# Kernel tuning notes

Measured on AMD Instinct MI355X. Metric: run time of the kernel, lower is better.

Reference implementation:

```python
import jax, jax.numpy as jnp
import numpy as np

TOP_K = 2


def setup_inputs() -> dict:
    key = jax.random.key(0)
    k0, k1, k2, k3, k4 = jax.random.split(key, 5)
    B, S, D, F, E = 4, 2048, 2048, 1408, 8
    scale = 0.02
    return {
        "hidden_states": jax.random.normal(k0, (B, S, D), jnp.float32),
        "router_w": jax.random.normal(k1, (D, E), jnp.float32) * scale,
        "w_gate": jax.random.normal(k2, (E, D, F), jnp.float32) * scale,
        "w_up": jax.random.normal(k3, (E, D, F), jnp.float32) * scale,
        "w_down": jax.random.normal(k4, (E, F, D), jnp.float32) * scale,
    }


def reference(hidden_states, router_w, w_gate, w_up, w_down):
    B, S, D = hidden_states.shape
    x = hidden_states.reshape(-1, D)              # [N, D]
    N = x.shape[0]
    E = router_w.shape[-1]

    # ---- Router: softmax over experts, top-k, renormalize top-k probs ----
    logits = x @ router_w                         # [N, E]
    probs = jax.nn.softmax(logits, axis=-1)
    top_w, top_i = jax.lax.top_k(probs, TOP_K)    # [N, K]
    top_w = top_w / jnp.sum(top_w, axis=-1, keepdims=True)

    # Dense gate matrix [N, E]: gate is the (renormalized) routing weight for
    # selected experts, zero otherwise.
    gates = jnp.zeros_like(probs).at[jnp.arange(N)[:, None], top_i].set(top_w)

    # ---- Load-balancing aux loss (Switch-style, averaged over top-k) ----
    f = jnp.mean(jnp.sum(jax.nn.one_hot(top_i, E, dtype=x.dtype), axis=1), axis=0)  # [E] dispatch fraction
    P = jnp.mean(probs, axis=0)                   # [E] mean router prob
    aux_loss = (E / TOP_K) * jnp.sum(f * P)

    # ---- Per-expert SwiGLU FFN, computed as grouped GEMMs over all experts ----
    g = jnp.einsum("nd,edf->enf", x, w_gate)      # [E, N, F]
    u = jnp.einsum("nd,edf->enf", x, w_up)        # [E, N, F]
    h = jax.nn.silu(g) * u                        # [E, N, F]
    expert_out = jnp.einsum("enf,efd->end", h, w_down)  # [E, N, D]

    # ---- Combine: gate-weighted sum over experts ----
    out = jnp.einsum("ne,end->nd", gates, expert_out)   # [N, D]
    return out.reshape(B, S, D), aux_loss
```

## Files before the change

kernel.cpp:

```cpp
#include <hip/hip_runtime.h>

#define N_TOK 8192
#define DIM   2048
#define FFN   1408

#define XB_OFF  0ull
#define HP_OFF  0ull
#define XGP_OFF 49020928ull
#define P1_OFF  120324096ull
#define EO_OFF  49020928ull
#define P2_OFF  212598784ull
#define LPK_OFF 258736128ull
#define TI_OFF  258801664ull
#define TW_OFF  258834432ull
#define TP_OFF  258867200ull
#define ST_OFF  258932736ull

typedef __bf16 bf16x8 __attribute__((ext_vector_type(8)));
typedef float  f32x4  __attribute__((ext_vector_type(4)));
typedef int    int4v  __attribute__((ext_vector_type(4)));
typedef __attribute__((address_space(1))) void as1_void;
typedef __attribute__((address_space(3))) void as3_void;

__device__ __forceinline__ void gload16(const void* g, void* l) {
  __builtin_amdgcn_global_load_lds((as1_void*)g, (as3_void*)l, 16, 0, 0);
}

__device__ __forceinline__ ushort f2bf(float f) {
  unsigned u = __builtin_bit_cast(unsigned, f);
  u += 0x7FFFu + ((u >> 16) & 1u);
  return (ushort)(u >> 16);
}

__device__ __forceinline__ int4v dsread(int addr) {
  int4v d;
  asm volatile("ds_read_b128 %0, %1" : "=v"(d) : "v"(addr));
  return d;
}

#define WAITL() do { asm volatile("s_waitcnt lgkmcnt(0)" ::: "memory"); \
                     __builtin_amdgcn_sched_barrier(0); } while (0)
#define BAR()   __builtin_amdgcn_s_barrier()
#define MFMA16(a, b, c) __builtin_amdgcn_mfma_f32_16x16x32_bf16(a, b, c, 0, 0, 0)
#define BC(x) __builtin_bit_cast(bf16x8, x)

__device__ __forceinline__ int swz(int row, int s) {
  int q = row >> 1;
  int p = (((row & 1) << 2) | s) ^ (q & 7);
  return q * 128 + p * 16;
}

__global__ __launch_bounds__(256) void router_kernel(
    const float* __restrict__ x, const float* __restrict__ rw,
    ushort* __restrict__ xb, int* __restrict__ topi, float* __restrict__ topw,
    int* __restrict__ cnt, unsigned long long* __restrict__ psum)
{
  int tid = threadIdx.x, lane = tid & 63, wv = tid >> 6;
  __shared__ float sP[4][8];
  __shared__ int   sC[4][8];
  float pacc[8]; int cacc[8];
  #pragma unroll
  for (int e = 0; e < 8; ++e) { pacc[e] = 0.f; cacc[e] = 0; }

  #pragma unroll 1
  for (int it = 0; it < 4; ++it) {
    int t = blockIdx.x * 16 + wv * 4 + it;
    const float4* xr = (const float4*)(x + (size_t)t * DIM);
    float acc[8];
    #pragma unroll
    for (int e = 0; e < 8; ++e) acc[e] = 0.f;
    #pragma unroll 1
    for (int i = 0; i < 8; ++i) {
      int j = i * 64 + lane;
      float4 v = xr[j];
      ushort4 o; o.x = f2bf(v.x); o.y = f2bf(v.y); o.z = f2bf(v.z); o.w = f2bf(v.w);
      *(ushort4*)(xb + (size_t)t * DIM + (size_t)j * 4) = o;
      const float* rr = rw + (size_t)j * 32;
      #pragma unroll
      for (int c = 0; c < 4; ++c) {
        float xv = (&v.x)[c];
        const float4* r4 = (const float4*)(rr + c * 8);
        float4 q0 = r4[0], q1 = r4[1];
        acc[0] += xv * q0.x; acc[1] += xv * q0.y; acc[2] += xv * q0.z; acc[3] += xv * q0.w;
        acc[4] += xv * q1.x; acc[5] += xv * q1.y; acc[6] += xv * q1.z; acc[7] += xv * q1.w;
      }
    }
    #pragma unroll
    for (int off = 32; off; off >>= 1) {
      #pragma unroll
      for (int e = 0; e < 8; ++e) acc[e] += __shfl_xor(acc[e], off);
    }
    float m = acc[0];
    #pragma unroll
    for (int e = 1; e < 8; ++e) m = fmaxf(m, acc[e]);
    float p[8], s = 0.f;
    #pragma unroll
    for (int e = 0; e < 8; ++e) { p[e] = __expf(acc[e] - m); s += p[e]; }
    float inv = 1.f / s;
    int i1 = 0; float p1 = p[0];
    #pragma unroll
    for (int e = 1; e < 8; ++e) if (p[e] > p1) { p1 = p[e]; i1 = e; }
    int i2 = -1; float p2 = -1.f;
    #pragma unroll
    for (int e = 0; e < 8; ++e) if (e != i1 && p[e] > p2) { p2 = p[e]; i2 = e; }
    float w1 = p1 / (p1 + p2);
    if (lane == 0) {
      topi[t] = i1 | (i2 << 8);
      topw[t] = w1;
      #pragma unroll
      for (int e = 0; e < 8; ++e) pacc[e] += p[e] * inv;
      cacc[i1]++; cacc[i2]++;
    }
  }
  if (lane == 0) {
    #pragma unroll
    for (int e = 0; e < 8; ++e) { sP[wv][e] = pacc[e]; sC[wv][e] = cacc[e]; }
  }
  __syncthreads();
  if (tid < 8) {
    float ps = sP[0][tid] + sP[1][tid] + sP[2][tid] + sP[3][tid];
    int   cs = sC[0][tid] + sC[1][tid] + sC[2][tid] + sC[3][tid];
    atomicAdd(&cnt[tid], cs);
    atomicAdd(&psum[tid], (unsigned long long)((double)ps * 1099511627776.0));
  }
}

__global__ void scan_aux_kernel(int* __restrict__ stats,
                                const unsigned long long* __restrict__ psum,
                                float* __restrict__ aux_out)
{
  if (threadIdx.x == 0 && blockIdx.x == 0) {
    int b = 0, tb = 0;
    for (int e = 0; e < 8; ++e) {
      stats[8 + e] = b; stats[16 + e] = b; stats[24 + e] = tb;
      tb += (stats[e] + 127) >> 7;
      b += stats[e];
    }
    stats[32] = tb;
    double s = 0.0;
    for (int e = 0; e < 8; ++e)
      s += (double)stats[e] * ((double)psum[e] * (1.0 / 1099511627776.0));
    aux_out[0] = (float)(4.0 * s / ((double)N_TOK * (double)N_TOK));
  }
}

__global__ __launch_bounds__(256) void place_kernel(
    const int* __restrict__ topi, int* __restrict__ stats,
    int* __restrict__ lpk, int2* __restrict__ tpos)
{
  int t = blockIdx.x * 256 + threadIdx.x;
  if (t >= N_TOK) return;
  int pk = topi[t];
  int e1 = pk & 0xff, e2 = (pk >> 8) & 0xff;
  int p1 = atomicAdd(&stats[8 + e1], 1);
  lpk[p1] = t;
  int p2 = atomicAdd(&stats[8 + e2], 1);
  lpk[p2] = t;
  tpos[t] = make_int2(p1, p2);
}

__global__ __launch_bounds__(256) void gather_x_kernel(
    const ushort* __restrict__ xb, const int* __restrict__ lpk,
    const int* __restrict__ stats, char* __restrict__ xgp)
{
  int b = blockIdx.x;
  if (b >= stats[32]) return;
  int e = 0;
  #pragma unroll
  for (int k = 1; k < 8; ++k) if (b >= stats[24 + k]) e = k;
  int tloc = b - stats[24 + e];
  int abase = stats[16 + e], Me = stats[e];
  int lane = threadIdx.x & 63, wv = threadIdx.x >> 6;
  char* base = xgp + (size_t)b * 64 * 8192;
  #pragma unroll 1
  for (int r = wv; r < 128; r += 4) {
    int lrow = tloc * 128 + r;
    bool valid = lrow < Me;
    const char* src = (const char*)xb + (valid ? (size_t)lpk[abase + lrow] * (DIM * 2) : 0);
    int q = r >> 1;
    #pragma unroll
    for (int it = 0; it < 4; ++it) {
      int c16 = it * 64 + lane;
      int j = c16 >> 2, s = c16 & 3;
      uint4 v;
      if (valid) v = *(const uint4*)(src + c16 * 16);
      else       v = make_uint4(0, 0, 0, 0);
      int p = (((r & 1) << 2) | s) ^ (q & 7);
      *(uint4*)(base + (size_t)j * 8192 + q * 128 + p * 16) = v;
    }
  }
}

__global__ __launch_bounds__(256) void pack_gu_kernel(
    const float* __restrict__ wg, const float* __restrict__ wu, char* __restrict__ p1)
{
  int j = blockIdx.x, tn = blockIdx.y, e = blockIdx.z;
  __shared__ float tg[32][65];
  __shared__ float tu[32][65];
  int t = threadIdx.x;
  const float* gs = wg + ((size_t)e * DIM + j * 32) * FFN + tn * 64;
  const float* us = wu + ((size_t)e * DIM + j * 32) * FFN + tn * 64;
  #pragma unroll
  for (int k2 = 0; k2 < 2; ++k2) {
    int idx = t + k2 * 256;
    int kk = idx >> 4, fq = idx & 15;
    *(float4*)&tg[kk][fq * 4] = *(const float4*)(gs + (size_t)kk * FFN + fq * 4);
    *(float4*)&tu[kk][fq * 4] = *(const float4*)(us + (size_t)kk * FFN + fq * 4);
  }
  __syncthreads();
  char* dst = p1 + ((size_t)((e * 22 + tn) * 64 + j)) * 8192;
  #pragma unroll
  for (int k2 = 0; k2 < 2; ++k2) {
    int L = t + k2 * 256;
    int q = L >> 3, v = (L & 7) ^ (q & 7);
    int r = 2 * q + (v >> 2), s = v & 3;
    const float* col = (r < 64) ? &tg[s * 8][r] : &tu[s * 8][r - 64];
    ushort u8[8];
    #pragma unroll
    for (int i = 0; i < 8; ++i) u8[i] = f2bf(col[i * 65]);
    *(ushort4*)(dst + (size_t)L * 16) = *(ushort4*)&u8[0];
    *(ushort4*)(dst + (size_t)L * 16 + 8) = *(ushort4*)&u8[4];
  }
}

__global__ __launch_bounds__(256) void pack_d_kernel(
    const float* __restrict__ wd, char* __restrict__ p2)
{
  int j = blockIdx.x, tn = blockIdx.y, e = blockIdx.z;
  __shared__ float t2[32][129];
  int t = threadIdx.x;
  const float* src = wd + ((size_t)e * FFN + j * 32) * DIM + tn * 128;
  #pragma unroll
  for (int k2 = 0; k2 < 4; ++k2) {
    int idx = t + k2 * 256;
    int kk = idx >> 5, dq = idx & 31;
    *(float4*)&t2[kk][dq * 4] = *(const float4*)(src + (size_t)kk * DIM + dq * 4);
  }
  __syncthreads();
  char* dst = p2 + ((size_t)((e * 16 + tn) * 44 + j)) * 8192;
  #pragma unroll
  for (int k2 = 0; k2 < 2; ++k2) {
    int L = t + k2 * 256;
    int q = L >> 3, v = (L & 7) ^ (q & 7);
    int r = 2 * q + (v >> 2), s = v & 3;
    ushort u8[8];
    #pragma unroll
    for (int i = 0; i < 8; ++i) u8[i] = f2bf(t2[s * 8 + i][r]);
    *(ushort4*)(dst + (size_t)L * 16) = *(ushort4*)&u8[0];
    *(ushort4*)(dst + (size_t)L * 16 + 8) = *(ushort4*)&u8[4];
  }
}


#define GSTAGE(AC, BC_, BUF) do { int d_ = (BUF) * 16384 + wv * 2048; \
  gload16((AC) + wv * 2048 + lane * 16, sm + d_); \
  gload16((AC) + wv * 2048 + 1024 + lane * 16, sm + d_ + 1024); \
  gload16((BC_) + wv * 2048 + lane * 16, sm + d_ + 8192); \
  gload16((BC_) + wv * 2048 + 1024 + lane * 16, sm + d_ + 8192 + 1024); \
} while (0)

#define KLOOP(NCH) \
  GSTAGE(aP, bP, 0); \
  _Pragma("unroll 1") \
  for (int j = 0; j < (NCH); ++j) { \
    if (j + 1 < (NCH)) { \
      GSTAGE(aP + (size_t)(j + 1) * 8192, bP + (size_t)(j + 1) * 8192, (j + 1) & 1); \
      asm volatile("s_waitcnt vmcnt(4)" ::: "memory"); \
    } else { \
      asm volatile("s_waitcnt vmcnt(0)" ::: "memory"); \
    } \
    BAR(); \
    int sb = (j & 1) * 16384; \
    int4v va[4], vb[4]; \
    _Pragma("unroll") for (int n = 0; n < 4; ++n) vb[n] = dsread(sb + adB[n]); \
    _Pragma("unroll") for (int m = 0; m < 4; ++m) va[m] = dsread(sb + adA[m]); \
    WAITL(); \
    __builtin_amdgcn_s_setprio(1); \
    _Pragma("unroll") for (int m = 0; m < 4; ++m) \
      _Pragma("unroll") for (int n = 0; n < 4; ++n) \
        acc[m][n] = MFMA16(BC(va[m]), BC(vb[n]), acc[m][n]); \
    __builtin_amdgcn_s_setprio(0); \
    BAR(); \
  }

__global__ __launch_bounds__(256, 4) void gemm_gu_kernel(
    const char* __restrict__ xgp, const char* __restrict__ p1,
    const int* __restrict__ stats, char* __restrict__ hp)
{
  int bid = blockIdx.x;
  int e = bid & 7;
  int Ll = bid >> 3;
  int tm = Ll / 22, tn = Ll % 22;
  int Me = stats[e];
  if (tm * 128 >= Me) return;
  int tb = stats[24 + e];

  __shared__ char sm[32768];
  int tid = threadIdx.x, lane = tid & 63, wv = tid >> 6;
  const char* aP = xgp + (size_t)(tb + tm) * 64 * 8192;
  const char* bP = p1 + (size_t)((e * 22 + tn) * 64) * 8192;

  int wm = wv >> 1, wn = wv & 1, s = lane >> 4;
  int adA[4], adB[4];
  #pragma unroll
  for (int m = 0; m < 4; ++m) adA[m] = swz(wm * 64 + m * 16 + (lane & 15), s);
  #pragma unroll
  for (int n = 0; n < 4; ++n) adB[n] = 8192 + swz(wn * 64 + n * 16 + (lane & 15), s);

  f32x4 acc[4][4];
  #pragma unroll
  for (int m = 0; m < 4; ++m)
    #pragma unroll
    for (int n = 0; n < 4; ++n) acc[m][n] = (f32x4){0, 0, 0, 0};

  KLOOP(64);

  float* u_lds = (float*)sm;
  if (wn == 1) {
    #pragma unroll
    for (int m = 0; m < 4; ++m)
      #pragma unroll
      for (int n = 0; n < 4; ++n)
        #pragma unroll
        for (int r = 0; r < 4; ++r) {
          int row = wm * 64 + m * 16 + (lane >> 4) * 4 + r;
          int c = n * 16 + (lane & 15);
          u_lds[row * 64 + c] = acc[m][n][r];
        }
  }
  __syncthreads();
  if (wn == 0) {
    char* hb = hp + (size_t)(tb + tm) * 44 * 8192;
    #pragma unroll
    for (int m = 0; m < 4; ++m)
      #pragma unroll
      for (int n = 0; n < 4; ++n)
        #pragma unroll
        for (int r = 0; r < 4; ++r) {
          int row = wm * 64 + m * 16 + (lane >> 4) * 4 + r;
          int c = n * 16 + (lane & 15);
          float g = acc[m][n][r];
          float u = u_lds[row * 64 + c];
          float hv = g * u / (1.f + __expf(-g));
          int f = tn * 64 + c;
          int j2 = f >> 5, s2 = (f >> 3) & 3, i2 = f & 7;
          int q = row >> 1;
          int p = (((row & 1) << 2) | s2) ^ (q & 7);
          *(ushort*)(hb + (size_t)j2 * 8192 + q * 128 + p * 16 + i2 * 2) = f2bf(hv);
        }
  }
}

__global__ __launch_bounds__(256, 4) void gemm_down_kernel(
    const char* __restrict__ hp, const char* __restrict__ p2,
    const int* __restrict__ stats, float* __restrict__ eo)
{
  int bid = blockIdx.x;
  int e = bid & 7;
  int Ll = bid >> 3;
  int tm = Ll >> 4, tn = Ll & 15;
  int Me = stats[e];
  if (tm * 128 >= Me) return;
  int tb = stats[24 + e], abase = stats[16 + e];

  __shared__ char sm[32768];
  int tid = threadIdx.x, lane = tid & 63, wv = tid >> 6;
  const char* aP = hp + (size_t)(tb + tm) * 44 * 8192;
  const char* bP = p2 + (size_t)((e * 16 + tn) * 44) * 8192;

  int wm = wv >> 1, wn = wv & 1, s = lane >> 4;
  int adA[4], adB[4];
  #pragma unroll
  for (int m = 0; m < 4; ++m) adA[m] = swz(wm * 64 + m * 16 + (lane & 15), s);
  #pragma unroll
  for (int n = 0; n < 4; ++n) adB[n] = 8192 + swz(wn * 64 + n * 16 + (lane & 15), s);

  f32x4 acc[4][4];
  #pragma unroll
  for (int m = 0; m < 4; ++m)
    #pragma unroll
    for (int n = 0; n < 4; ++n) acc[m][n] = (f32x4){0, 0, 0, 0};

  KLOOP(44);

  int c0 = lane & 15, r0 = (lane >> 4) * 4;
  #pragma unroll
  for (int m = 0; m < 4; ++m) {
    #pragma unroll
    for (int r = 0; r < 4; ++r) {
      int lrow = tm * 128 + wm * 64 + m * 16 + r0 + r;
      if (lrow < Me) {
        float* dst = eo + (size_t)(abase + lrow) * DIM + tn * 128 + wn * 64 + c0;
        #pragma unroll
        for (int n = 0; n < 4; ++n) dst[n * 16] = acc[m][n][r];
      }
    }
  }
}

__global__ __launch_bounds__(256) void combine_kernel(
    const float* __restrict__ eo, const int2* __restrict__ tpos,
    const float* __restrict__ topw, float* __restrict__ out)
{
  int t = blockIdx.x;
  int2 tp = tpos[t];
  float w1 = topw[t], w2 = 1.f - w1;
  const float4* r1 = (const float4*)(eo + (size_t)tp.x * DIM);
  const float4* r2 = (const float4*)(eo + (size_t)tp.y * DIM);
  float4* o = (float4*)(out + (size_t)t * DIM);
  #pragma unroll
  for (int k = 0; k < 2; ++k) {
    int i = threadIdx.x + k * 256;
    float4 a = r1[i], b = r2[i];
    float4 c;
    c.x = w1 * a.x + w2 * b.x;
    c.y = w1 * a.y + w2 * b.y;
    c.z = w1 * a.z + w2 * b.z;
    c.w = w1 * a.w + w2 * b.w;
    o[i] = c;
  }
}

extern "C" void kernel_launch(void* const* d_in, const int* in_sizes, int n_in,
                              void* d_out, int out_size, void* d_ws, size_t ws_size,
                              hipStream_t stream)
{
  const float* x  = (const float*)d_in[0];
  const float* rw = (const float*)d_in[1];
  const float* wg = (const float*)d_in[2];
  const float* wu = (const float*)d_in[3];
  const float* wd = (const float*)d_in[4];
  float* out = (float*)d_out;

  char* ws = (char*)d_ws;
  ushort* xb   = (ushort*)(ws + XB_OFF);
  char*   hp   = ws + HP_OFF;
  char*   xgp  = ws + XGP_OFF;
  char*   p1   = ws + P1_OFF;
  float*  eo   = (float*)(ws + EO_OFF);
  char*   p2   = ws + P2_OFF;
  int*    lpk  = (int*)(ws + LPK_OFF);
  int*    topi = (int*)(ws + TI_OFF);
  float*  topw = (float*)(ws + TW_OFF);
  int2*   tpos = (int2*)(ws + TP_OFF);
  int*    stats = (int*)(ws + ST_OFF);
  unsigned long long* psum = (unsigned long long*)(ws + ST_OFF + 192);

  hipMemsetAsync(ws + ST_OFF, 0, 256, stream);

  router_kernel<<<512, 256, 0, stream>>>(x, rw, xb, topi, topw, stats, psum);
  scan_aux_kernel<<<1, 64, 0, stream>>>(stats, psum, out + (size_t)out_size - 1);
  place_kernel<<<32, 256, 0, stream>>>(topi, stats, lpk, tpos);

  gather_x_kernel<<<136, 256, 0, stream>>>(xb, lpk, stats, xgp);
  pack_gu_kernel<<<dim3(64, 22, 8), 256, 0, stream>>>(wg, wu, p1);
  pack_d_kernel<<<dim3(44, 16, 8), 256, 0, stream>>>(wd, p2);

  gemm_gu_kernel<<<5632, 256, 0, stream>>>(xgp, p1, stats, hp);
  gemm_down_kernel<<<4096, 256, 0, stream>>>(hp, p2, stats, eo);

  combine_kernel<<<8192, 256, 0, stream>>>(eo, tpos, topw, out);
}
```

Measured before the change: 581.9 us.

## Enlarge GEMM tiles to 256x128 with 8 waves and 4-stage LDS pipeline

Both expert GEMMs move from 128x128 tiles with 4 waves to 256-row tiles with 8 waves per block, 128KB of dynamic LDS and a 4-buffer prefetch ring. Global loads are interleaved between MFMA sub-phases so they overlap compute. The packed weight and gathered-activation layouts, the block counts, and the workspace offsets are all updated to 16KB K-chunks, and pack_d now runs after the first GEMM so its buffer can alias p1. The aim is more data reuse per block and better latency hiding, at the cost of occupancy dropping to one block per CU. The grid sizes are oversized, so many blocks exit early.

```diff
diff --git a/kernel.cpp b/kernel.cpp
--- a/kernel.cpp
+++ b/kernel.cpp
@@ -4,17 +4,17 @@
 #define DIM   2048
 #define FFN   1408
 
-#define XB_OFF  0ull
 #define HP_OFF  0ull
-#define XGP_OFF 49020928ull
-#define P1_OFF  120324096ull
-#define EO_OFF  49020928ull
-#define P2_OFF  212598784ull
-#define LPK_OFF 258736128ull
-#define TI_OFF  258801664ull
-#define TW_OFF  258834432ull
-#define TP_OFF  258867200ull
-#define ST_OFF  258932736ull
+#define XB_OFF  51183616ull
+#define P1_OFF  51183616ull
+#define P2_OFF  51183616ull
+#define EO_OFF  97320960ull
+#define XGP_OFF 143458304ull
+#define LPK_OFF 231538688ull
+#define TI_OFF  231604224ull
+#define TW_OFF  231636992ull
+#define TP_OFF  231669760ull
+#define ST_OFF  231735296ull
 
 typedef __bf16 bf16x8 __attribute__((ext_vector_type(8)));
 typedef float  f32x4  __attribute__((ext_vector_type(4)));
@@ -133,7 +133,7 @@
     int b = 0, tb = 0;
     for (int e = 0; e < 8; ++e) {
       stats[8 + e] = b; stats[16 + e] = b; stats[24 + e] = tb;
-      tb += (stats[e] + 127) >> 7;
+      tb += (stats[e] + 255) >> 8;
       b += stats[e];
     }
     stats[32] = tb;
@@ -170,24 +170,34 @@
   for (int k = 1; k < 8; ++k) if (b >= stats[24 + k]) e = k;
   int tloc = b - stats[24 + e];
   int abase = stats[16 + e], Me = stats[e];
-  int lane = threadIdx.x & 63, wv = threadIdx.x >> 6;
-  char* base = xgp + (size_t)b * 64 * 8192;
+
+  int r = threadIdx.x;
+  int lrow = tloc * 256 + r;
+  bool valid = lrow < Me;
+  const char* src = (const char*)xb + (valid ? (size_t)lpk[abase + lrow] * (DIM * 2) : 0);
+  char* base = xgp + (size_t)b * (64 * 16384);
+  int q = r >> 1;
+  int p0 = (((r & 1) << 2) | 0) ^ (q & 7);
+  int p1_ = (((r & 1) << 2) | 1) ^ (q & 7);
+  int p2_ = (((r & 1) << 2) | 2) ^ (q & 7);
+  int p3 = (((r & 1) << 2) | 3) ^ (q & 7);
+
   #pragma unroll 1
-  for (int r = wv; r < 128; r += 4) {
-    int lrow = tloc * 128 + r;
-    bool valid = lrow < Me;
-    const char* src = (const char*)xb + (valid ? (size_t)lpk[abase + lrow] * (DIM * 2) : 0);
-    int q = r >> 1;
-    #pragma unroll
-    for (int it = 0; it < 4; ++it) {
-      int c16 = it * 64 + lane;
-      int j = c16 >> 2, s = c16 & 3;
-      uint4 v;
-      if (valid) v = *(const uint4*)(src + c16 * 16);
-      else       v = make_uint4(0, 0, 0, 0);
-      int p = (((r & 1) << 2) | s) ^ (q & 7);
-      *(uint4*)(base + (size_t)j * 8192 + q * 128 + p * 16) = v;
-    }
+  for (int j = 0; j < 64; ++j) {
+    uint4 v0, v1, v2, v3;
+    if (valid) {
+      v0 = *(const uint4*)(src + j * 64);
+      v1 = *(const uint4*)(src + j * 64 + 16);
+      v2 = *(const uint4*)(src + j * 64 + 32);
+      v3 = *(const uint4*)(src + j * 64 + 48);
+    } else {
+      v0 = v1 = v2 = v3 = make_uint4(0, 0, 0, 0);
+    }
+    char* u = base + (size_t)j * 16384 + q * 128;
+    *(uint4*)(u + p0 * 16) = v0;
+    *(uint4*)(u + p1_ * 16) = v1;
+    *(uint4*)(u + p2_ * 16) = v2;
+    *(uint4*)(u + p3 * 16) = v3;
   }
 }
 
@@ -195,29 +205,33 @@
     const float* __restrict__ wg, const float* __restrict__ wu, char* __restrict__ p1)
 {
   int j = blockIdx.x, tn = blockIdx.y, e = blockIdx.z;
-  __shared__ float tg[32][65];
-  __shared__ float tu[32][65];
+  __shared__ float tg[32][129];
+  __shared__ float tu[32][129];
   int t = threadIdx.x;
-  const float* gs = wg + ((size_t)e * DIM + j * 32) * FFN + tn * 64;
-  const float* us = wu + ((size_t)e * DIM + j * 32) * FFN + tn * 64;
-  #pragma unroll
-  for (int k2 = 0; k2 < 2; ++k2) {
+  const float* gs = wg + ((size_t)e * DIM + j * 32) * FFN + tn * 128;
+  const float* us = wu + ((size_t)e * DIM + j * 32) * FFN + tn * 128;
+  #pragma unroll
+  for (int k2 = 0; k2 < 4; ++k2) {
     int idx = t + k2 * 256;
-    int kk = idx >> 4, fq = idx & 15;
+    int kk = idx >> 5, fq = idx & 31;
     *(float4*)&tg[kk][fq * 4] = *(const float4*)(gs + (size_t)kk * FFN + fq * 4);
     *(float4*)&tu[kk][fq * 4] = *(const float4*)(us + (size_t)kk * FFN + fq * 4);
   }
   __syncthreads();
-  char* dst = p1 + ((size_t)((e * 22 + tn) * 64 + j)) * 8192;
-  #pragma unroll
-  for (int k2 = 0; k2 < 2; ++k2) {
+  char* dst = p1 + ((size_t)((e * 11 + tn) * 64 + j)) * 16384;
+  #pragma unroll
+  for (int k2 = 0; k2 < 4; ++k2) {
     int L = t + k2 * 256;
     int q = L >> 3, v = (L & 7) ^ (q & 7);
-    int r = 2 * q + (v >> 2), s = v & 3;
-    const float* col = (r < 64) ? &tg[s * 8][r] : &tu[s * 8][r - 64];
+    int row = 2 * q + (v >> 2), s = v & 3;
     ushort u8[8];
-    #pragma unroll
-    for (int i = 0; i < 8; ++i) u8[i] = f2bf(col[i * 65]);
+    if (row < 128) {
+      #pragma unroll
+      for (int i = 0; i < 8; ++i) u8[i] = f2bf(tg[s * 8 + i][row]);
+    } else {
+      #pragma unroll
+      for (int i = 0; i < 8; ++i) u8[i] = f2bf(tu[s * 8 + i][row - 128]);
+    }
     *(ushort4*)(dst + (size_t)L * 16) = *(ushort4*)&u8[0];
     *(ushort4*)(dst + (size_t)L * 16 + 8) = *(ushort4*)&u8[4];
   }
@@ -227,157 +241,184 @@
     const float* __restrict__ wd, char* __restrict__ p2)
 {
   int j = blockIdx.x, tn = blockIdx.y, e = blockIdx.z;
-  __shared__ float t2[32][129];
+  __shared__ float t2[32][257];
   int t = threadIdx.x;
-  const float* src = wd + ((size_t)e * FFN + j * 32) * DIM + tn * 128;
+  const float* src = wd + ((size_t)e * FFN + j * 32) * DIM + tn * 256;
+  #pragma unroll
+  for (int k2 = 0; k2 < 8; ++k2) {
+    int idx = t + k2 * 256;
+    int kk = idx >> 6, dq = idx & 63;
+    *(float4*)&t2[kk][dq * 4] = *(const float4*)(src + (size_t)kk * DIM + dq * 4);
+  }
+  __syncthreads();
+  char* dst = p2 + ((size_t)((e * 8 + tn) * 44 + j)) * 16384;
   #pragma unroll
   for (int k2 = 0; k2 < 4; ++k2) {
-    int idx = t + k2 * 256;
-    int kk = idx >> 5, dq = idx & 31;
-    *(float4*)&t2[kk][dq * 4] = *(const float4*)(src + (size_t)kk * DIM + dq * 4);
-  }
-  __syncthreads();
-  char* dst = p2 + ((size_t)((e * 16 + tn) * 44 + j)) * 8192;
-  #pragma unroll
-  for (int k2 = 0; k2 < 2; ++k2) {
     int L = t + k2 * 256;
     int q = L >> 3, v = (L & 7) ^ (q & 7);
-    int r = 2 * q + (v >> 2), s = v & 3;
+    int row = 2 * q + (v >> 2), s = v & 3;
     ushort u8[8];
     #pragma unroll
-    for (int i = 0; i < 8; ++i) u8[i] = f2bf(t2[s * 8 + i][r]);
+    for (int i = 0; i < 8; ++i) u8[i] = f2bf(t2[s * 8 + i][row]);
     *(ushort4*)(dst + (size_t)L * 16) = *(ushort4*)&u8[0];
     *(ushort4*)(dst + (size_t)L * 16 + 8) = *(ushort4*)&u8[4];
   }
 }
 
 
-#define GSTAGE(AC, BC_, BUF) do { int d_ = (BUF) * 16384 + wv * 2048; \
-  gload16((AC) + wv * 2048 + lane * 16, sm + d_); \
-  gload16((AC) + wv * 2048 + 1024 + lane * 16, sm + d_ + 1024); \
-  gload16((BC_) + wv * 2048 + lane * 16, sm + d_ + 8192); \
-  gload16((BC_) + wv * 2048 + 1024 + lane * 16, sm + d_ + 8192 + 1024); \
-} while (0)
+#define STG(PTR, J, OFS, LOFS) \
+  gload16((PTR) + (size_t)(J) * 16384 + wv * 2048 + lane * 16 + (OFS), \
+          sm + ((J) & 3) * 32768 + (LOFS) + wv * 2048 + (OFS))
 
 #define KLOOP(NCH) \
-  GSTAGE(aP, bP, 0); \
+  _Pragma("unroll") \
+  for (int t_ = 0; t_ < 3; ++t_) { \
+    STG(aP, t_, 0, 0); STG(aP, t_, 1024, 0); \
+    STG(bP, t_, 0, 16384); STG(bP, t_, 1024, 16384); \
+  } \
   _Pragma("unroll 1") \
   for (int j = 0; j < (NCH); ++j) { \
-    if (j + 1 < (NCH)) { \
-      GSTAGE(aP + (size_t)(j + 1) * 8192, bP + (size_t)(j + 1) * 8192, (j + 1) & 1); \
-      asm volatile("s_waitcnt vmcnt(4)" ::: "memory"); \
-    } else { \
-      asm volatile("s_waitcnt vmcnt(0)" ::: "memory"); \
-    } \
+    if (j < (NCH) - 2)       asm volatile("s_waitcnt vmcnt(8)" ::: "memory"); \
+    else if (j == (NCH) - 2) asm volatile("s_waitcnt vmcnt(4)" ::: "memory"); \
+    else                     asm volatile("s_waitcnt vmcnt(0)" ::: "memory"); \
     BAR(); \
-    int sb = (j & 1) * 16384; \
-    int4v va[4], vb[4]; \
-    _Pragma("unroll") for (int n = 0; n < 4; ++n) vb[n] = dsread(sb + adB[n]); \
+    int sb = (j & 3) * 32768; \
+    bool pf = (j + 3 < (NCH)); \
+    int4v va[8], vb[4]; \
+     \
+    if (pf) STG(aP, j + 3, 0, 0); \
     _Pragma("unroll") for (int m = 0; m < 4; ++m) va[m] = dsread(sb + adA[m]); \
+    vb[0] = dsread(sb + adB[0]); vb[1] = dsread(sb + adB[1]); \
     WAITL(); \
     __builtin_amdgcn_s_setprio(1); \
-    _Pragma("unroll") for (int m = 0; m < 4; ++m) \
-      _Pragma("unroll") for (int n = 0; n < 4; ++n) \
-        acc[m][n] = MFMA16(BC(va[m]), BC(vb[n]), acc[m][n]); \
+    _Pragma("unroll") for (int m = 0; m < 4; ++m) { \
+      acc[m][0] = MFMA16(BC(va[m]), BC(vb[0]), acc[m][0]); \
+      acc[m][1] = MFMA16(BC(va[m]), BC(vb[1]), acc[m][1]); } \
+    __builtin_amdgcn_s_setprio(0); \
+     \
+    if (pf) STG(aP, j + 3, 1024, 0); \
+    vb[2] = dsread(sb + adB[2]); vb[3] = dsread(sb + adB[3]); \
+    WAITL(); \
+    __builtin_amdgcn_s_setprio(1); \
+    _Pragma("unroll") for (int m = 0; m < 4; ++m) { \
+      acc[m][2] = MFMA16(BC(va[m]), BC(vb[2]), acc[m][2]); \
+      acc[m][3] = MFMA16(BC(va[m]), BC(vb[3]), acc[m][3]); } \
+    __builtin_amdgcn_s_setprio(0); \
+     \
+    if (pf) STG(bP, j + 3, 0, 16384); \
+    _Pragma("unroll") for (int m = 0; m < 4; ++m) va[4 + m] = dsread(sb + adA[4 + m]); \
+    WAITL(); \
+    __builtin_amdgcn_s_setprio(1); \
+    _Pragma("unroll") for (int m = 0; m < 4; ++m) { \
+      acc[4 + m][0] = MFMA16(BC(va[4 + m]), BC(vb[0]), acc[4 + m][0]); \
+      acc[4 + m][1] = MFMA16(BC(va[4 + m]), BC(vb[1]), acc[4 + m][1]); } \
+    __builtin_amdgcn_s_setprio(0); \
+     \
+    if (pf) STG(bP, j + 3, 1024, 16384); \
+    __builtin_amdgcn_s_setprio(1); \
+    _Pragma("unroll") for (int m = 0; m < 4; ++m) { \
+      acc[4 + m][2] = MFMA16(BC(va[4 + m]), BC(vb[2]), acc[4 + m][2]); \
+      acc[4 + m][3] = MFMA16(BC(va[4 + m]), BC(vb[3]), acc[4 + m][3]); } \
     __builtin_amdgcn_s_setprio(0); \
     BAR(); \
   }
 
-__global__ __launch_bounds__(256, 4) void gemm_gu_kernel(
+__global__ __launch_bounds__(512, 1) void gemm_gu_kernel(
     const char* __restrict__ xgp, const char* __restrict__ p1,
     const int* __restrict__ stats, char* __restrict__ hp)
 {
   int bid = blockIdx.x;
   int e = bid & 7;
   int Ll = bid >> 3;
-  int tm = Ll / 22, tn = Ll % 22;
+  int tm = Ll / 11, tn = Ll % 11;
   int Me = stats[e];
-  if (tm * 128 >= Me) return;
+  if (tm * 256 >= Me) return;
   int tb = stats[24 + e];
 
-  __shared__ char sm[32768];
+  extern __shared__ char sm[];
   int tid = threadIdx.x, lane = tid & 63, wv = tid >> 6;
-  const char* aP = xgp + (size_t)(tb + tm) * 64 * 8192;
-  const char* bP = p1 + (size_t)((e * 22 + tn) * 64) * 8192;
-
-  int wm = wv >> 1, wn = wv & 1, s = lane >> 4;
-  int adA[4], adB[4];
-  #pragma unroll
-  for (int m = 0; m < 4; ++m) adA[m] = swz(wm * 64 + m * 16 + (lane & 15), s);
-  #pragma unroll
-  for (int n = 0; n < 4; ++n) adB[n] = 8192 + swz(wn * 64 + n * 16 + (lane & 15), s);
-
-  f32x4 acc[4][4];
-  #pragma unroll
-  for (int m = 0; m < 4; ++m)
+  const char* aP = xgp + (size_t)(tb + tm) * 64 * 16384;
+  const char* bP = p1 + (size_t)((e * 11 + tn) * 64) * 16384;
+
+  int wm = wv >> 2, wn = wv & 3, s = lane >> 4;
+  int adA[8], adB[4];
+  #pragma unroll
+  for (int m = 0; m < 8; ++m) adA[m] = swz(wm * 128 + m * 16 + (lane & 15), s);
+  #pragma unroll
+  for (int n = 0; n < 4; ++n) adB[n] = 16384 + swz(wn * 64 + n * 16 + (lane & 15), s);
+
+  f32x4 acc[8][4];
+  #pragma unroll
+  for (int m = 0; m < 8; ++m)
     #pragma unroll
     for (int n = 0; n < 4; ++n) acc[m][n] = (f32x4){0, 0, 0, 0};
 
   KLOOP(64);
 
+  __syncthreads();
   float* u_lds = (float*)sm;
-  if (wn == 1) {
-    #pragma unroll
-    for (int m = 0; m < 4; ++m)
+  if (wn >= 2) {
+    #pragma unroll
+    for (int m = 0; m < 8; ++m)
       #pragma unroll
       for (int n = 0; n < 4; ++n)
         #pragma unroll
         for (int r = 0; r < 4; ++r) {
-          int row = wm * 64 + m * 16 + (lane >> 4) * 4 + r;
-          int c = n * 16 + (lane & 15);
-          u_lds[row * 64 + c] = acc[m][n][r];
+          int row = wm * 128 + m * 16 + (lane >> 4) * 4 + r;
+          int fc = (wn - 2) * 64 + n * 16 + (lane & 15);
+          u_lds[row * 128 + fc] = acc[m][n][r];
         }
   }
   __syncthreads();
-  if (wn == 0) {
-    char* hb = hp + (size_t)(tb + tm) * 44 * 8192;
-    #pragma unroll
-    for (int m = 0; m < 4; ++m)
+  if (wn < 2) {
+    char* hb = hp + (size_t)(tb + tm) * 44 * 16384;
+    #pragma unroll
+    for (int m = 0; m < 8; ++m)
       #pragma unroll
       for (int n = 0; n < 4; ++n)
         #pragma unroll
         for (int r = 0; r < 4; ++r) {
-          int row = wm * 64 + m * 16 + (lane >> 4) * 4 + r;
-          int c = n * 16 + (lane & 15);
+          int row = wm * 128 + m * 16 + (lane >> 4) * 4 + r;
+          int fc = wn * 64 + n * 16 + (lane & 15);
           float g = acc[m][n][r];
-          float u = u_lds[row * 64 + c];
+          float u = u_lds[row * 128 + fc];
           float hv = g * u / (1.f + __expf(-g));
-          int f = tn * 64 + c;
+          int f = tn * 128 + fc;
           int j2 = f >> 5, s2 = (f >> 3) & 3, i2 = f & 7;
           int q = row >> 1;
           int p = (((row & 1) << 2) | s2) ^ (q & 7);
-          *(ushort*)(hb + (size_t)j2 * 8192 + q * 128 + p * 16 + i2 * 2) = f2bf(hv);
+          *(ushort*)(hb + (size_t)j2 * 16384 + q * 128 + p * 16 + i2 * 2) = f2bf(hv);
         }
   }
 }
 
-__global__ __launch_bounds__(256, 4) void gemm_down_kernel(
+__global__ __launch_bounds__(512, 1) void gemm_down_kernel(
     const char* __restrict__ hp, const char* __restrict__ p2,
     const int* __restrict__ stats, float* __restrict__ eo)
 {
   int bid = blockIdx.x;
   int e = bid & 7;
   int Ll = bid >> 3;
-  int tm = Ll >> 4, tn = Ll & 15;
+  int tm = Ll >> 3, tn = Ll & 7;
   int Me = stats[e];
-  if (tm * 128 >= Me) return;
+  if (tm * 256 >= Me) return;
   int tb = stats[24 + e], abase = stats[16 + e];
 
-  __shared__ char sm[32768];
+  extern __shared__ char sm[];
   int tid = threadIdx.x, lane = tid & 63, wv = tid >> 6;
-  const char* aP = hp + (size_t)(tb + tm) * 44 * 8192;
-  const char* bP = p2 + (size_t)((e * 16 + tn) * 44) * 8192;
-
-  int wm = wv >> 1, wn = wv & 1, s = lane >> 4;
-  int adA[4], adB[4];
-  #pragma unroll
-  for (int m = 0; m < 4; ++m) adA[m] = swz(wm * 64 + m * 16 + (lane & 15), s);
-  #pragma unroll
-  for (int n = 0; n < 4; ++n) adB[n] = 8192 + swz(wn * 64 + n * 16 + (lane & 15), s);
-
-  f32x4 acc[4][4];
-  #pragma unroll
-  for (int m = 0; m < 4; ++m)
+  const char* aP = hp + (size_t)(tb + tm) * 44 * 16384;
+  const char* bP = p2 + (size_t)((e * 8 + tn) * 44) * 16384;
+
+  int wm = wv >> 2, wn = wv & 3, s = lane >> 4;
+  int adA[8], adB[4];
+  #pragma unroll
+  for (int m = 0; m < 8; ++m) adA[m] = swz(wm * 128 + m * 16 + (lane & 15), s);
+  #pragma unroll
+  for (int n = 0; n < 4; ++n) adB[n] = 16384 + swz(wn * 64 + n * 16 + (lane & 15), s);
+
+  f32x4 acc[8][4];
+  #pragma unroll
+  for (int m = 0; m < 8; ++m)
     #pragma unroll
     for (int n = 0; n < 4; ++n) acc[m][n] = (f32x4){0, 0, 0, 0};
 
@@ -385,12 +426,12 @@
 
   int c0 = lane & 15, r0 = (lane >> 4) * 4;
   #pragma unroll
-  for (int m = 0; m < 4; ++m) {
+  for (int m = 0; m < 8; ++m) {
     #pragma unroll
     for (int r = 0; r < 4; ++r) {
-      int lrow = tm * 128 + wm * 64 + m * 16 + r0 + r;
+      int lrow = tm * 256 + wm * 128 + m * 16 + r0 + r;
       if (lrow < Me) {
-        float* dst = eo + (size_t)(abase + lrow) * DIM + tn * 128 + wn * 64 + c0;
+        float* dst = eo + (size_t)(abase + lrow) * DIM + tn * 256 + wn * 64 + c0;
         #pragma unroll
         for (int n = 0; n < 4; ++n) dst[n * 16] = acc[m][n][r];
       }
@@ -433,12 +474,12 @@
   float* out = (float*)d_out;
 
   char* ws = (char*)d_ws;
+  char*   hp   = ws + HP_OFF;
   ushort* xb   = (ushort*)(ws + XB_OFF);
-  char*   hp   = ws + HP_OFF;
+  char*   p1   = ws + P1_OFF;
+  char*   p2   = ws + P2_OFF;
+  float*  eo   = (float*)(ws + EO_OFF);
   char*   xgp  = ws + XGP_OFF;
-  char*   p1   = ws + P1_OFF;
-  float*  eo   = (float*)(ws + EO_OFF);
-  char*   p2   = ws + P2_OFF;
   int*    lpk  = (int*)(ws + LPK_OFF);
   int*    topi = (int*)(ws + TI_OFF);
   float*  topw = (float*)(ws + TW_OFF);
@@ -452,12 +493,14 @@
   scan_aux_kernel<<<1, 64, 0, stream>>>(stats, psum, out + (size_t)out_size - 1);
   place_kernel<<<32, 256, 0, stream>>>(topi, stats, lpk, tpos);
 
-  gather_x_kernel<<<136, 256, 0, stream>>>(xb, lpk, stats, xgp);
-  pack_gu_kernel<<<dim3(64, 22, 8), 256, 0, stream>>>(wg, wu, p1);
-  pack_d_kernel<<<dim3(44, 16, 8), 256, 0, stream>>>(wd, p2);
-
-  gemm_gu_kernel<<<5632, 256, 0, stream>>>(xgp, p1, stats, hp);
-  gemm_down_kernel<<<4096, 256, 0, stream>>>(hp, p2, stats, eo);
+  gather_x_kernel<<<71, 256, 0, stream>>>(xb, lpk, stats, xgp);
+  pack_gu_kernel<<<dim3(64, 11, 8), 256, 0, stream>>>(wg, wu, p1);
+
+  gemm_gu_kernel<<<5632, 512, 131072, stream>>>(xgp, p1, stats, hp);
+
+  pack_d_kernel<<<dim3(44, 8, 8), 256, 0, stream>>>(wd, p2);
+
+  gemm_down_kernel<<<4096, 512, 131072, stream>>>(hp, p2, stats, eo);
 
   combine_kernel<<<8192, 256, 0, stream>>>(eo, tpos, topw, out);
 }
```

Result: slower. 683.2 us (+17.4%).

## Fuse router and weight packing into one prep kernel, bf16 expert outputs

Applied to the files above, without the earlier changes.

Merges the router, gate/up weight pack and down weight pack into a single block-indexed prep kernel, so the router's small grid overlaps with the large packing work and two launches go away. Doubles the gather grid by splitting each 128-row tile across two blocks for more parallelism. Stores the down-projection expert outputs as bf16 instead of fp32 and widens the combine loads to match, halving that intermediate's write and read traffic at the cost of extra rounding on the output.

```diff
diff --git a/kernel.cpp b/kernel.cpp
--- a/kernel.cpp
+++ b/kernel.cpp
@@ -7,8 +7,8 @@
 #define XB_OFF  0ull
 #define HP_OFF  0ull
 #define XGP_OFF 49020928ull
+#define EO_OFF  49020928ull
 #define P1_OFF  120324096ull
-#define EO_OFF  49020928ull
 #define P2_OFF  212598784ull
 #define LPK_OFF 258736128ull
 #define TI_OFF  258801664ull
@@ -31,6 +31,8 @@
   u += 0x7FFFu + ((u >> 16) & 1u);
   return (ushort)(u >> 16);
 }
+__device__ __forceinline__ float blo(unsigned w) { return __builtin_bit_cast(float, w << 16); }
+__device__ __forceinline__ float bhi(unsigned w) { return __builtin_bit_cast(float, w & 0xffff0000u); }
 
 __device__ __forceinline__ int4v dsread(int addr) {
   int4v d;
@@ -50,78 +52,141 @@
   return q * 128 + p * 16;
 }
 
-__global__ __launch_bounds__(256) void router_kernel(
+__global__ __launch_bounds__(256) void prep_kernel(
     const float* __restrict__ x, const float* __restrict__ rw,
     ushort* __restrict__ xb, int* __restrict__ topi, float* __restrict__ topw,
-    int* __restrict__ cnt, unsigned long long* __restrict__ psum)
-{
-  int tid = threadIdx.x, lane = tid & 63, wv = tid >> 6;
-  __shared__ float sP[4][8];
-  __shared__ int   sC[4][8];
-  float pacc[8]; int cacc[8];
-  #pragma unroll
-  for (int e = 0; e < 8; ++e) { pacc[e] = 0.f; cacc[e] = 0; }
-
-  #pragma unroll 1
-  for (int it = 0; it < 4; ++it) {
-    int t = blockIdx.x * 16 + wv * 4 + it;
-    const float4* xr = (const float4*)(x + (size_t)t * DIM);
-    float acc[8];
-    #pragma unroll
-    for (int e = 0; e < 8; ++e) acc[e] = 0.f;
+    int* __restrict__ cnt, unsigned long long* __restrict__ psum,
+    const float* __restrict__ wg, const float* __restrict__ wu,
+    const float* __restrict__ wd, char* __restrict__ p1, char* __restrict__ p2)
+{
+  __shared__ char smem[16640];
+  int b = blockIdx.x;
+
+  if (b < 512) {
+    int tid = threadIdx.x, lane = tid & 63, wv = tid >> 6;
+    float (*sP)[8] = (float(*)[8])smem;
+    int   (*sC)[8] = (int(*)[8])(smem + 128);
+    float pacc[8]; int cacc[8];
+    #pragma unroll
+    for (int e = 0; e < 8; ++e) { pacc[e] = 0.f; cacc[e] = 0; }
+
     #pragma unroll 1
-    for (int i = 0; i < 8; ++i) {
-      int j = i * 64 + lane;
-      float4 v = xr[j];
-      ushort4 o; o.x = f2bf(v.x); o.y = f2bf(v.y); o.z = f2bf(v.z); o.w = f2bf(v.w);
-      *(ushort4*)(xb + (size_t)t * DIM + (size_t)j * 4) = o;
-      const float* rr = rw + (size_t)j * 32;
-      #pragma unroll
-      for (int c = 0; c < 4; ++c) {
-        float xv = (&v.x)[c];
-        const float4* r4 = (const float4*)(rr + c * 8);
-        float4 q0 = r4[0], q1 = r4[1];
-        acc[0] += xv * q0.x; acc[1] += xv * q0.y; acc[2] += xv * q0.z; acc[3] += xv * q0.w;
-        acc[4] += xv * q1.x; acc[5] += xv * q1.y; acc[6] += xv * q1.z; acc[7] += xv * q1.w;
+    for (int it = 0; it < 4; ++it) {
+      int t = b * 16 + wv * 4 + it;
+      const float4* xr = (const float4*)(x + (size_t)t * DIM);
+      float acc[8];
+      #pragma unroll
+      for (int e = 0; e < 8; ++e) acc[e] = 0.f;
+      #pragma unroll 1
+      for (int i = 0; i < 8; ++i) {
+        int j = i * 64 + lane;
+        float4 v = xr[j];
+        ushort4 o; o.x = f2bf(v.x); o.y = f2bf(v.y); o.z = f2bf(v.z); o.w = f2bf(v.w);
+        *(ushort4*)(xb + (size_t)t * DIM + (size_t)j * 4) = o;
+        const float* rr = rw + (size_t)j * 32;
+        #pragma unroll
+        for (int c = 0; c < 4; ++c) {
+          float xv = (&v.x)[c];
+          const float4* r4 = (const float4*)(rr + c * 8);
+          float4 q0 = r4[0], q1 = r4[1];
+          acc[0] += xv * q0.x; acc[1] += xv * q0.y; acc[2] += xv * q0.z; acc[3] += xv * q0.w;
+          acc[4] += xv * q1.x; acc[5] += xv * q1.y; acc[6] += xv * q1.z; acc[7] += xv * q1.w;
+        }
       }
-    }
-    #pragma unroll
-    for (int off = 32; off; off >>= 1) {
-      #pragma unroll
-      for (int e = 0; e < 8; ++e) acc[e] += __shfl_xor(acc[e], off);
-    }
-    float m = acc[0];
-    #pragma unroll
-    for (int e = 1; e < 8; ++e) m = fmaxf(m, acc[e]);
-    float p[8], s = 0.f;
-    #pragma unroll
-    for (int e = 0; e < 8; ++e) { p[e] = __expf(acc[e] - m); s += p[e]; }
-    float inv = 1.f / s;
-    int i1 = 0; float p1 = p[0];
-    #pragma unroll
-    for (int e = 1; e < 8; ++e) if (p[e] > p1) { p1 = p[e]; i1 = e; }
-    int i2 = -1; float p2 = -1.f;
-    #pragma unroll
-    for (int e = 0; e < 8; ++e) if (e != i1 && p[e] > p2) { p2 = p[e]; i2 = e; }
-    float w1 = p1 / (p1 + p2);
+      #pragma unroll
+      for (int off = 32; off; off >>= 1) {
+        #pragma unroll
+        for (int e = 0; e < 8; ++e) acc[e] += __shfl_xor(acc[e], off);
+      }
+      float m = acc[0];
+      #pragma unroll
+      for (int e = 1; e < 8; ++e) m = fmaxf(m, acc[e]);
+      float p[8], s = 0.f;
+      #pragma unroll
+      for (int e = 0; e < 8; ++e) { p[e] = __expf(acc[e] - m); s += p[e]; }
+      float inv = 1.f / s;
+      int i1 = 0; float p1v = p[0];
+      #pragma unroll
+      for (int e = 1; e < 8; ++e) if (p[e] > p1v) { p1v = p[e]; i1 = e; }
+      int i2 = -1; float p2v = -1.f;
+      #pragma unroll
+      for (int e = 0; e < 8; ++e) if (e != i1 && p[e] > p2v) { p2v = p[e]; i2 = e; }
+      float w1 = p1v / (p1v + p2v);
+      if (lane == 0) {
+        topi[t] = i1 | (i2 << 8);
+        topw[t] = w1;
+        #pragma unroll
+        for (int e = 0; e < 8; ++e) pacc[e] += p[e] * inv;
+        cacc[i1]++; cacc[i2]++;
+      }
+    }
     if (lane == 0) {
-      topi[t] = i1 | (i2 << 8);
-      topw[t] = w1;
-      #pragma unroll
-      for (int e = 0; e < 8; ++e) pacc[e] += p[e] * inv;
-      cacc[i1]++; cacc[i2]++;
-    }
-  }
-  if (lane == 0) {
-    #pragma unroll
-    for (int e = 0; e < 8; ++e) { sP[wv][e] = pacc[e]; sC[wv][e] = cacc[e]; }
-  }
-  __syncthreads();
-  if (tid < 8) {
-    float ps = sP[0][tid] + sP[1][tid] + sP[2][tid] + sP[3][tid];
-    int   cs = sC[0][tid] + sC[1][tid] + sC[2][tid] + sC[3][tid];
-    atomicAdd(&cnt[tid], cs);
-    atomicAdd(&psum[tid], (unsigned long long)((double)ps * 1099511627776.0));
+      #pragma unroll
+      for (int e = 0; e < 8; ++e) { sP[wv][e] = pacc[e]; sC[wv][e] = cacc[e]; }
+    }
+    __syncthreads();
+    if (tid < 8) {
+      float ps = sP[0][tid] + sP[1][tid] + sP[2][tid] + sP[3][tid];
+      int   cs = sC[0][tid] + sC[1][tid] + sC[2][tid] + sC[3][tid];
+      atomicAdd(&cnt[tid], cs);
+      atomicAdd(&psum[tid], (unsigned long long)((double)ps * 1099511627776.0));
+    }
+  } else if (b < 11776) {
+    int q_ = b - 512;
+    int j = q_ & 63, rest = q_ >> 6;
+    int tn = rest % 22, e = rest / 22;
+    float (*tg)[65] = (float(*)[65])smem;
+    float (*tu)[65] = (float(*)[65])(smem + 8320);
+    int t = threadIdx.x;
+    const float* gs = wg + ((size_t)e * DIM + j * 32) * FFN + tn * 64;
+    const float* us = wu + ((size_t)e * DIM + j * 32) * FFN + tn * 64;
+    #pragma unroll
+    for (int k2 = 0; k2 < 2; ++k2) {
+      int idx = t + k2 * 256;
+      int kk = idx >> 4, fq = idx & 15;
+      *(float4*)&tg[kk][fq * 4] = *(const float4*)(gs + (size_t)kk * FFN + fq * 4);
+      *(float4*)&tu[kk][fq * 4] = *(const float4*)(us + (size_t)kk * FFN + fq * 4);
+    }
+    __syncthreads();
+    char* dst = p1 + ((size_t)((e * 22 + tn) * 64 + j)) * 8192;
+    #pragma unroll
+    for (int k2 = 0; k2 < 2; ++k2) {
+      int L = t + k2 * 256;
+      int q = L >> 3, v = (L & 7) ^ (q & 7);
+      int r = 2 * q + (v >> 2), s = v & 3;
+      const float* col = (r < 64) ? &tg[s * 8][r] : &tu[s * 8][r - 64];
+      ushort u8[8];
+      #pragma unroll
+      for (int i = 0; i < 8; ++i) u8[i] = f2bf(col[i * 65]);
+      *(ushort4*)(dst + (size_t)L * 16) = *(ushort4*)&u8[0];
+      *(ushort4*)(dst + (size_t)L * 16 + 8) = *(ushort4*)&u8[4];
+    }
+  } else {
+    int q_ = b - 11776;
+    int j = q_ % 44, rest = q_ / 44;
+    int tn = rest & 15, e = rest >> 4;
+    float (*t2)[129] = (float(*)[129])smem;
+    int t = threadIdx.x;
+    const float* src = wd + ((size_t)e * FFN + j * 32) * DIM + tn * 128;
+    #pragma unroll
+    for (int k2 = 0; k2 < 4; ++k2) {
+      int idx = t + k2 * 256;
+      int kk = idx >> 5, dq = idx & 31;
+      *(float4*)&t2[kk][dq * 4] = *(const float4*)(src + (size_t)kk * DIM + dq * 4);
+    }
+    __syncthreads();
+    char* dst = p2 + ((size_t)((e * 16 + tn) * 44 + j)) * 8192;
+    #pragma unroll
+    for (int k2 = 0; k2 < 2; ++k2) {
+      int L = t + k2 * 256;
+      int q = L >> 3, v = (L & 7) ^ (q & 7);
+      int r = 2 * q + (v >> 2), s = v & 3;
+      ushort u8[8];
+      #pragma unroll
+      for (int i = 0; i < 8; ++i) u8[i] = f2bf(t2[s * 8 + i][r]);
+      *(ushort4*)(dst + (size_t)L * 16) = *(ushort4*)&u8[0];
+      *(ushort4*)(dst + (size_t)L * 16 + 8) = *(ushort4*)&u8[4];
+    }
   }
 }
 
@@ -164,16 +229,18 @@
     const int* __restrict__ stats, char* __restrict__ xgp)
 {
   int b = blockIdx.x;
-  if (b >= stats[32]) return;
+  int tile = b >> 1;
+  if (tile >= stats[32]) return;
   int e = 0;
   #pragma unroll
-  for (int k = 1; k < 8; ++k) if (b >= stats[24 + k]) e = k;
-  int tloc = b - stats[24 + e];
+  for (int k = 1; k < 8; ++k) if (tile >= stats[24 + k]) e = k;
+  int tloc = tile - stats[24 + e];
   int abase = stats[16 + e], Me = stats[e];
+  int half = b & 1;
   int lane = threadIdx.x & 63, wv = threadIdx.x >> 6;
-  char* base = xgp + (size_t)b * 64 * 8192;
+  char* base = xgp + (size_t)tile * 64 * 8192;
   #pragma unroll 1
-  for (int r = wv; r < 128; r += 4) {
+  for (int r = half * 64 + wv; r < half * 64 + 64; r += 4) {
     int lrow = tloc * 128 + r;
     bool valid = lrow < Me;
     const char* src = (const char*)xb + (valid ? (size_t)lpk[abase + lrow] * (DIM * 2) : 0);
@@ -188,66 +255,6 @@
       int p = (((r & 1) << 2) | s) ^ (q & 7);
       *(uint4*)(base + (size_t)j * 8192 + q * 128 + p * 16) = v;
     }
-  }
-}
-
-__global__ __launch_bounds__(256) void pack_gu_kernel(
-    const float* __restrict__ wg, const float* __restrict__ wu, char* __restrict__ p1)
-{
-  int j = blockIdx.x, tn = blockIdx.y, e = blockIdx.z;
-  __shared__ float tg[32][65];
-  __shared__ float tu[32][65];
-  int t = threadIdx.x;
-  const float* gs = wg + ((size_t)e * DIM + j * 32) * FFN + tn * 64;
-  const float* us = wu + ((size_t)e * DIM + j * 32) * FFN + tn * 64;
-  #pragma unroll
-  for (int k2 = 0; k2 < 2; ++k2) {
-    int idx = t + k2 * 256;
-    int kk = idx >> 4, fq = idx & 15;
-    *(float4*)&tg[kk][fq * 4] = *(const float4*)(gs + (size_t)kk * FFN + fq * 4);
-    *(float4*)&tu[kk][fq * 4] = *(const float4*)(us + (size_t)kk * FFN + fq * 4);
-  }
-  __syncthreads();
-  char* dst = p1 + ((size_t)((e * 22 + tn) * 64 + j)) * 8192;
-  #pragma unroll
-  for (int k2 = 0; k2 < 2; ++k2) {
-    int L = t + k2 * 256;
-    int q = L >> 3, v = (L & 7) ^ (q & 7);
-    int r = 2 * q + (v >> 2), s = v & 3;
-    const float* col = (r < 64) ? &tg[s * 8][r] : &tu[s * 8][r - 64];
-    ushort u8[8];
-    #pragma unroll
-    for (int i = 0; i < 8; ++i) u8[i] = f2bf(col[i * 65]);
-    *(ushort4*)(dst + (size_t)L * 16) = *(ushort4*)&u8[0];
-    *(ushort4*)(dst + (size_t)L * 16 + 8) = *(ushort4*)&u8[4];
-  }
-}
-
-__global__ __launch_bounds__(256) void pack_d_kernel(
-    const float* __restrict__ wd, char* __restrict__ p2)
-{
-  int j = blockIdx.x, tn = blockIdx.y, e = blockIdx.z;
-  __shared__ float t2[32][129];
-  int t = threadIdx.x;
-  const float* src = wd + ((size_t)e * FFN + j * 32) * DIM + tn * 128;
-  #pragma unroll
-  for (int k2 = 0; k2 < 4; ++k2) {
-    int idx = t + k2 * 256;
-    int kk = idx >> 5, dq = idx & 31;
-    *(float4*)&t2[kk][dq * 4] = *(const float4*)(src + (size_t)kk * DIM + dq * 4);
-  }
-  __syncthreads();
-  char* dst = p2 + ((size_t)((e * 16 + tn) * 44 + j)) * 8192;
-  #pragma unroll
-  for (int k2 = 0; k2 < 2; ++k2) {
-    int L = t + k2 * 256;
-    int q = L >> 3, v = (L & 7) ^ (q & 7);
-    int r = 2 * q + (v >> 2), s = v & 3;
-    ushort u8[8];
-    #pragma unroll
-    for (int i = 0; i < 8; ++i) u8[i] = f2bf(t2[s * 8 + i][r]);
-    *(ushort4*)(dst + (size_t)L * 16) = *(ushort4*)&u8[0];
-    *(ushort4*)(dst + (size_t)L * 16 + 8) = *(ushort4*)&u8[4];
   }
 }
 
@@ -353,7 +360,7 @@
 
 __global__ __launch_bounds__(256, 4) void gemm_down_kernel(
     const char* __restrict__ hp, const char* __restrict__ p2,
-    const int* __restrict__ stats, float* __restrict__ eo)
+    const int* __restrict__ stats, ushort* __restrict__ eo)
 {
   int bid = blockIdx.x;
   int e = bid & 7;
@@ -390,35 +397,33 @@
     for (int r = 0; r < 4; ++r) {
       int lrow = tm * 128 + wm * 64 + m * 16 + r0 + r;
       if (lrow < Me) {
-        float* dst = eo + (size_t)(abase + lrow) * DIM + tn * 128 + wn * 64 + c0;
-        #pragma unroll
-        for (int n = 0; n < 4; ++n) dst[n * 16] = acc[m][n][r];
+        ushort* dst = eo + (size_t)(abase + lrow) * DIM + tn * 128 + wn * 64 + c0;
+        #pragma unroll
+        for (int n = 0; n < 4; ++n) dst[n * 16] = f2bf(acc[m][n][r]);
       }
     }
   }
 }
 
 __global__ __launch_bounds__(256) void combine_kernel(
-    const float* __restrict__ eo, const int2* __restrict__ tpos,
+    const ushort* __restrict__ eo, const int2* __restrict__ tpos,
     const float* __restrict__ topw, float* __restrict__ out)
 {
   int t = blockIdx.x;
   int2 tp = tpos[t];
   float w1 = topw[t], w2 = 1.f - w1;
-  const float4* r1 = (const float4*)(eo + (size_t)tp.x * DIM);
-  const float4* r2 = (const float4*)(eo + (size_t)tp.y * DIM);
+  const uint4* r1 = (const uint4*)(eo + (size_t)tp.x * DIM);
+  const uint4* r2 = (const uint4*)(eo + (size_t)tp.y * DIM);
   float4* o = (float4*)(out + (size_t)t * DIM);
-  #pragma unroll
-  for (int k = 0; k < 2; ++k) {
-    int i = threadIdx.x + k * 256;
-    float4 a = r1[i], b = r2[i];
-    float4 c;
-    c.x = w1 * a.x + w2 * b.x;
-    c.y = w1 * a.y + w2 * b.y;
-    c.z = w1 * a.z + w2 * b.z;
-    c.w = w1 * a.w + w2 * b.w;
-    o[i] = c;
-  }
+  int i = threadIdx.x;
+  uint4 a = r1[i], b = r2[i];
+  float4 c0, c1;
+  c0.x = w1 * blo(a.x) + w2 * blo(b.x);  c0.y = w1 * bhi(a.x) + w2 * bhi(b.x);
+  c0.z = w1 * blo(a.y) + w2 * blo(b.y);  c0.w = w1 * bhi(a.y) + w2 * bhi(b.y);
+  c1.x = w1 * blo(a.z) + w2 * blo(b.z);  c1.y = w1 * bhi(a.z) + w2 * bhi(b.z);
+  c1.z = w1 * blo(a.w) + w2 * blo(b.w);  c1.w = w1 * bhi(a.w) + w2 * bhi(b.w);
+  o[i * 2] = c0;
+  o[i * 2 + 1] = c1;
 }
 
 extern "C" void kernel_launch(void* const* d_in, const int* in_sizes, int n_in,
@@ -436,8 +441,8 @@
   ushort* xb   = (ushort*)(ws + XB_OFF);
   char*   hp   = ws + HP_OFF;
   char*   xgp  = ws + XGP_OFF;
+  ushort* eo   = (ushort*)(ws + EO_OFF);
   char*   p1   = ws + P1_OFF;
-  float*  eo   = (float*)(ws + EO_OFF);
   char*   p2   = ws + P2_OFF;
   int*    lpk  = (int*)(ws + LPK_OFF);
   int*    topi = (int*)(ws + TI_OFF);
@@ -448,13 +453,12 @@
 
   hipMemsetAsync(ws + ST_OFF, 0, 256, stream);
 
-  router_kernel<<<512, 256, 0, stream>>>(x, rw, xb, topi, topw, stats, psum);
+  prep_kernel<<<17408, 256, 0, stream>>>(x, rw, xb, topi, topw, stats, psum,
+                                         wg, wu, wd, p1, p2);
   scan_aux_kernel<<<1, 64, 0, stream>>>(stats, psum, out + (size_t)out_size - 1);
   place_kernel<<<32, 256, 0, stream>>>(topi, stats, lpk, tpos);
 
-  gather_x_kernel<<<136, 256, 0, stream>>>(xb, lpk, stats, xgp);
-  pack_gu_kernel<<<dim3(64, 22, 8), 256, 0, stream>>>(wg, wu, p1);
-  pack_d_kernel<<<dim3(44, 16, 8), 256, 0, stream>>>(wd, p2);
+  gather_x_kernel<<<272, 256, 0, stream>>>(xb, lpk, stats, xgp);
 
   gemm_gu_kernel<<<5632, 256, 0, stream>>>(xgp, p1, stats, hp);
   gemm_down_kernel<<<4096, 256, 0, stream>>>(hp, p2, stats, eo);
```

Result: faster. 534.5 us (-8.2%).
